# Kernel optimization log

Measured on AMD Instinct MI355X. Metric: run time of the kernel, lower is better.

## Reference

```python
import jax, jax.numpy as jnp
from jax import lax
import numpy as np

B, T = 128, 270
NS = 8            # non-spatial features per step
IH = IW = 64      # spatial precip map
H_LSTM = 256
POOL = 4


def setup_inputs() -> dict:
    key = jax.random.key(0)
    ks = jax.random.split(key, 16)
    r = lambda k, s, sc=0.05: (jax.random.normal(k, s, dtype=jnp.float32) * sc)
    return {
        "x": jax.random.normal(ks[0], (B, T, NS + IH * IW), dtype=jnp.float32),
        "conv1_w": r(ks[1], (2, 1, 3, 3), 0.3),
        "conv1_b": r(ks[2], (2,)),
        "conv2_w": r(ks[3], (4, 2, 3, 3), 0.3),
        "conv2_b": r(ks[4], (4,)),
        "fc_w": r(ks[5], (8, 36), 0.2),
        "fc_b": r(ks[6], (8,)),
        "w_ih": r(ks[7], (4 * H_LSTM, NS + 8), 0.2),
        "w_hh": r(ks[8], (4 * H_LSTM, H_LSTM), 0.06),
        "b_ih": r(ks[9], (4 * H_LSTM,)),
        "b_hh": r(ks[10], (4 * H_LSTM,)),
        "head_w": r(ks[11], (1, H_LSTM), 0.06),
        "head_b": r(ks[12], (1,)),
        "h0": jax.random.normal(ks[13], (B, H_LSTM), dtype=jnp.float32),
        "c0": jax.random.normal(ks[14], (B, H_LSTM), dtype=jnp.float32),
    }


def _conv(z, w, b):
    y = lax.conv_general_dilated(z, w, (1, 1), "VALID",
                                 dimension_numbers=("NCHW", "OIHW", "NCHW"))
    return y + b[None, :, None, None]


def _maxpool(z):
    return lax.reduce_window(z, -jnp.inf, lax.max,
                             (1, 1, POOL, POOL), (1, 1, POOL, POOL), "VALID")


def reference(x, conv1_w, conv1_b, conv2_w, conv2_b, fc_w, fc_b,
              w_ih, w_hh, b_ih, b_hh, head_w, head_b, h0, c0):
    bsz = x.shape[0]
    xs = jnp.swapaxes(x, 0, 1)  # [T, B, NS + IH*IW]

    def step(carry, xt):
        h, c = carry
        x_sp = xt[:, NS:].reshape(bsz, 1, IH, IW)   # spatial precip map
        x_ns = xt[:, :NS]                           # non-spatial features
        o = _maxpool(jax.nn.relu(_conv(x_sp, conv1_w, conv1_b)))
        o = _maxpool(jax.nn.relu(_conv(o, conv2_w, conv2_b)))
        o = o.reshape(bsz, -1) @ fc_w.T + fc_b      # [B, 8]
        inp = jnp.concatenate([x_ns, o], axis=1)    # [B, NS+8]
        gates = inp @ w_ih.T + b_ih + h @ w_hh.T + b_hh  # [B, 4H]
        i, f, g, og = jnp.split(gates, 4, axis=1)   # torch LSTMCell gate order
        c_new = jax.nn.sigmoid(f) * c + jax.nn.sigmoid(i) * jnp.tanh(g)
        h_new = jax.nn.sigmoid(og) * jnp.tanh(c_new)
        return (h_new, c_new), h_new

    _, hs = lax.scan(step, (h0, c0), xs)            # hs: [T, B, H]
    out = jnp.swapaxes(hs, 0, 1) @ head_w.T + head_b  # [B, T, 1]; dropout = eval mode
    return out
```

## Files before the change

kernel.cpp:

```cpp
#include <hip/hip_runtime.h>

#define B_ 128
#define T_ 270
#define XR 4104
#define H_ 256

typedef __attribute__((ext_vector_type(8))) short short8v;
typedef __attribute__((ext_vector_type(4))) float f32x4;

__device__ inline unsigned short f2bf(float f) {
  unsigned u = __builtin_bit_cast(unsigned, f);
  u += 0x7fffu + ((u >> 16) & 1u);
  return (unsigned short)(u >> 16);
}
__device__ inline float sigm(float x) { return 1.0f / (1.0f + __expf(-x)); }
__device__ inline float tanh_f(float x) {
  float t = __expf(-2.0f * fabsf(x));
  float r = (1.0f - t) / (1.0f + t);
  return copysignf(r, x);
}
__device__ inline short8v pack8(const float* p) {
  float4 a = *(const float4*)p, b = *(const float4*)(p + 4);
  short8v v;
  v[0] = (short)f2bf(a.x); v[1] = (short)f2bf(a.y);
  v[2] = (short)f2bf(a.z); v[3] = (short)f2bf(a.w);
  v[4] = (short)f2bf(b.x); v[5] = (short)f2bf(b.y);
  v[6] = (short)f2bf(b.z); v[7] = (short)f2bf(b.w);
  return v;
}
__device__ inline short8v pinned(short8v v) {
  union { short8v s; float f[4]; } u;
  u.s = v;
  asm volatile("" : "+v"(u.f[0]), "+v"(u.f[1]), "+v"(u.f[2]), "+v"(u.f[3]));
  return u.s;
}
#define MFMA(a, b, c) __builtin_amdgcn_mfma_f32_16x16x32_bf16((a), (b), (c), 0, 0, 0)

#define FEAT16_B ((size_t)T_ * B_ * 16 * 2)
#define SPACK_B  ((size_t)8 * 8 * 9 * 64 * 8 * 2)
#define HB_B     ((size_t)2 * 16 * 16 * 128 * 2)
#define HP_B     ((size_t)2 * 16 * 16 * 4 * 4)
#define FLAGS_B  ((size_t)16 * 16 * 4)
#define WS_NEED  (FEAT16_B + SPACK_B + HB_B + HP_B + FLAGS_B)

__global__ __launch_bounds__(256) void cnn_kernel(
    const float* __restrict__ x,
    const float* __restrict__ c1w_, const float* __restrict__ c1b_,
    const float* __restrict__ c2w_, const float* __restrict__ c2b_,
    const float* __restrict__ fcw, const float* __restrict__ fcb,
    unsigned short* __restrict__ feat16, unsigned* __restrict__ flags)
{
  __shared__ float img[64 * 68];
  __shared__ float p1[2 * 15 * 16];
  __shared__ float p2[36];
  __shared__ float wsm[96];
  const int tid = threadIdx.x;
  const int bt = blockIdx.x;
  const int b = bt & 127, t = bt >> 7;

  if (bt == 0 && tid < 16)
    __hip_atomic_store(flags + tid * 16, 0u, __ATOMIC_RELAXED, __HIP_MEMORY_SCOPE_AGENT);

  const float* src = x + ((long)b * T_ + t) * XR;

  if (tid < 18) wsm[tid] = c1w_[tid];
  else if (tid < 20) wsm[tid] = c1b_[tid - 18];
  else if (tid < 92) wsm[tid] = c2w_[tid - 20];
  else if (tid < 96) wsm[tid] = c2b_[tid - 92];

  {
    const float4* s4 = (const float4*)(src + 8);
#pragma unroll
    for (int i0 = 0; i0 < 4; i0++) {
      int i = tid + i0 * 256;
      float4 v = s4[i];
      int e = i * 4;
      *((float4*)&img[(e >> 6) * 68 + (e & 63)]) = v;
    }
  }
  __syncthreads();

  if (tid < 225) {
    int py = tid / 15, px = tid - (tid / 15) * 15;
    float w0[9], w1[9];
#pragma unroll
    for (int j = 0; j < 9; j++) { w0[j] = wsm[j]; w1[j] = wsm[9 + j]; }
    const float b0 = wsm[18], b1v = wsm[19];
    float m0 = -1e30f, m1 = -1e30f;
    for (int dy = 0; dy < 4; dy++) {
      for (int dx = 0; dx < 4; dx++) {
        const float* ip = &img[(py * 4 + dy) * 68 + px * 4 + dx];
        float s0 = b0, s1 = b1v;
#pragma unroll
        for (int ky = 0; ky < 3; ky++) {
#pragma unroll
          for (int kx = 0; kx < 3; kx++) {
            float v = ip[ky * 68 + kx];
            s0 = fmaf(v, w0[ky * 3 + kx], s0);
            s1 = fmaf(v, w1[ky * 3 + kx], s1);
          }
        }
        m0 = fmaxf(m0, s0); m1 = fmaxf(m1, s1);
      }
    }
    p1[py * 16 + px] = fmaxf(m0, 0.f);
    p1[240 + py * 16 + px] = fmaxf(m1, 0.f);
  }
  __syncthreads();

  if (tid < 36) {
    int ch = tid / 9, rem = tid - ch * 9;
    int py = rem / 3, px = rem - py * 3;
    float m = -1e30f;
    for (int dy = 0; dy < 4; dy++) {
      for (int dx = 0; dx < 4; dx++) {
        int y = py * 4 + dy, xx = px * 4 + dx;
        float s = wsm[92 + ch];
#pragma unroll
        for (int ic = 0; ic < 2; ic++)
#pragma unroll
          for (int ky = 0; ky < 3; ky++)
#pragma unroll
            for (int kx = 0; kx < 3; kx++)
              s = fmaf(p1[ic * 240 + (y + ky) * 16 + xx + kx],
                       wsm[20 + ((ch * 2 + ic) * 3 + ky) * 3 + kx], s);
        m = fmaxf(m, s);
      }
    }
    p2[tid] = fmaxf(m, 0.f);
  }
  __syncthreads();

  unsigned short* fr = feat16 + ((long)t * B_ + b) * 16;
  if (tid < 8) {
    float s = fcb[tid];
#pragma unroll
    for (int j = 0; j < 36; j++) s = fmaf(p2[j], fcw[tid * 36 + j], s);
    fr[8 + tid] = f2bf(s);
  } else if (tid < 16) {
    fr[tid - 8] = f2bf(src[tid - 8]);
  }
}

__global__ __launch_bounds__(256) void pack_kernel(
    const float* __restrict__ whh, const float* __restrict__ wih,
    unsigned short* __restrict__ spack)
{
  const int idx = blockIdx.x * 256 + threadIdx.x;
  if (idx >= 8 * 8 * 9 * 64) return;
  const int lane = idx & 63;
  const int fragid = idx >> 6;
  const int s = fragid % 9;
  const int uw = fragid / 9;
  const int u = uw & 7;
  const int hw_ = uw >> 3;
  const int hbk = hw_ >> 2, w = hw_ & 3;
  const int col15 = lane & 15, ko8 = (lane >> 4) * 8;
  const int col = (u >> 1) * 256 + hbk * 128 + w * 32 + (u & 1) * 16 + col15;
  short8v v = {0, 0, 0, 0, 0, 0, 0, 0};
  if (s < 8) {
    const int kf = (s < 4) ? (4 * hbk + s) : (4 * (1 - hbk) + (s - 4));
    v = pack8(whh + col * 256 + kf * 32 + ko8);
  } else if (ko8 < 16) {
    v = pack8(wih + col * 16 + ko8);
  }
  *(short8v*)(spack + (size_t)idx * 8) = v;
}

__global__ __launch_bounds__(256, 1) void lstm_kernel(
    const unsigned short* __restrict__ feat16,
    const float* __restrict__ bih, const float* __restrict__ bhh,
    const float* __restrict__ h0, const float* __restrict__ c0,
    const float* __restrict__ hw, const float* __restrict__ hdb,
    const unsigned short* __restrict__ spack,
    unsigned short* hb16, float* hpg, unsigned* flags,
    float* __restrict__ out)
{
  __shared__ __attribute__((aligned(16))) unsigned short hls[16 * 136];
  __shared__ float hpw[4 * 16];
  const int tid = threadIdx.x;
  const int w = tid >> 6, lane = tid & 63;
  const int gb = blockIdx.x & 7, hbk = blockIdx.x >> 3;
  const int gid = gb * 2 + hbk, pgid = gb * 2 + (1 - hbk);
  const int R0 = gb * 16, D0 = hbk * 128;
  const int col15 = lane & 15, ko8 = (lane >> 4) * 8, rb = (lane >> 4) * 4;
  const int Dl = w * 32;
  const int ar = col15;

  unsigned short* hbB[2] = { hb16, hb16 + 32768 };

  const unsigned short* sbase =
      spack + (size_t)((hbk * 4 + w) * 8) * 9 * 512 + (size_t)lane * 8;
#define SFRAG(u, s) (*(const short8v*)(sbase + ((u) * 9 + (s)) * 512))
  short8v bfO[4][8], bfP[4][8], bfF[8];
#pragma unroll
  for (int u = 0; u < 8; u++) {
#pragma unroll
    for (int s = 0; s < 4; s++) bfO[s][u] = pinned(SFRAG(u, s));
#pragma unroll
    for (int s = 0; s < 4; s++) bfP[s][u] = pinned(SFRAG(u, 4 + s));
    bfF[u] = pinned(SFRAG(u, 8));
  }

  float bsr[8];
#pragma unroll
  for (int u = 0; u < 8; u++) {
    const int col = (u >> 1) * 256 + D0 + Dl + (u & 1) * 16 + col15;
    bsr[u] = bih[col] + bhh[col];
  }
  float hwr[2] = { hw[D0 + Dl + col15], hw[D0 + Dl + 16 + col15] };
  const float hdb0 = hdb[0];

  float cs[2][4];
#pragma unroll
  for (int q = 0; q < 2; q++)
#pragma unroll
    for (int rr = 0; rr < 4; rr++) {
      const int row = rb + rr, dloc = Dl + q * 16 + col15;
      cs[q][rr] = c0[(R0 + row) * H_ + D0 + dloc];
      unsigned short hv = f2bf(h0[(R0 + row) * H_ + D0 + dloc]);
      hls[row * 136 + dloc] = hv;
      __hip_atomic_store(hbB[0] + (gid * 16 + row) * 128 + dloc, hv,
                         __ATOMIC_RELAXED, __HIP_MEMORY_SCOPE_AGENT);
    }
  __syncthreads();
  if (tid == 0)
    __hip_atomic_store(flags + gid * 16, 1u, __ATOMIC_RELEASE, __HIP_MEMORY_SCOPE_AGENT);

  const unsigned* pflag = flags + pgid * 16;

  for (int t = 0; t < T_; t++) {
    short8v af8 = (short8v){0, 0, 0, 0, 0, 0, 0, 0};
    if (ko8 < 16)
      af8 = *(const short8v*)(feat16 + ((size_t)t * B_ + R0 + ar) * 16 + ko8);

    f32x4 acc[8];
#pragma unroll
    for (int u = 0; u < 8; u++) acc[u] = (f32x4){0.f, 0.f, 0.f, 0.f};
#pragma unroll
    for (int s = 0; s < 4; s++) {
      short8v a = *(const short8v*)&hls[ar * 136 + s * 32 + ko8];
#pragma unroll
      for (int u = 0; u < 8; u++) acc[u] = MFMA(a, bfO[s][u], acc[u]);
    }
#pragma unroll
    for (int u = 0; u < 8; u++) acc[u] = MFMA(af8, bfF[u], acc[u]);

    {
      const unsigned need = (unsigned)(t + 1);
      unsigned v; long guard = 0;
      do {
        v = __hip_atomic_load(pflag, __ATOMIC_RELAXED, __HIP_MEMORY_SCOPE_AGENT);
      } while (v < need && ++guard < (1L << 22));
      __builtin_amdgcn_fence(__ATOMIC_ACQUIRE, "agent");
    }

    if (hbk == 0 && tid < 16 && t > 0) {
      float s = hdb0 + hpw[tid] + hpw[16 + tid] + hpw[32 + tid] + hpw[48 + tid];
      const float* pp = hpg + (t & 1) * 1024 + pgid * 64 + tid * 4;
#pragma unroll
      for (int i = 0; i < 4; i++)
        s += __hip_atomic_load(pp + i, __ATOMIC_RELAXED, __HIP_MEMORY_SCOPE_AGENT);
      out[(long)(R0 + tid) * T_ + (t - 1)] = s;
    }

    const unsigned long long* hbr = (const unsigned long long*)hbB[t & 1];
    unsigned long long pq[8];
#pragma unroll
    for (int s = 0; s < 4; s++) {
      const unsigned long long* pr =
          hbr + (size_t)(pgid * 16 + ar) * 32 + s * 8 + (ko8 >> 2);
      pq[2 * s]     = __hip_atomic_load(pr,     __ATOMIC_RELAXED, __HIP_MEMORY_SCOPE_AGENT);
      pq[2 * s + 1] = __hip_atomic_load(pr + 1, __ATOMIC_RELAXED, __HIP_MEMORY_SCOPE_AGENT);
    }
#pragma unroll
    for (int s = 0; s < 4; s++) {
      union { unsigned long long q[2]; short8v v; } u_;
      u_.q[0] = pq[2 * s]; u_.q[1] = pq[2 * s + 1];
#pragma unroll
      for (int u = 0; u < 8; u++) acc[u] = MFMA(u_.v, bfP[s][u], acc[u]);
    }

    __syncthreads();

    unsigned short* hbw = hbB[(t + 1) & 1];
    float ps[4] = {0.f, 0.f, 0.f, 0.f};
#pragma unroll
    for (int q = 0; q < 2; q++)
#pragma unroll
      for (int rr = 0; rr < 4; rr++) {
        float i_ = acc[0 + q][rr] + bsr[0 + q];
        float f_ = acc[2 + q][rr] + bsr[2 + q];
        float g_ = acc[4 + q][rr] + bsr[4 + q];
        float o_ = acc[6 + q][rr] + bsr[6 + q];
        float cn = sigm(f_) * cs[q][rr] + sigm(i_) * tanh_f(g_);
        cs[q][rr] = cn;
        float hn = sigm(o_) * tanh_f(cn);
        const int row = rb + rr, dloc = Dl + q * 16 + col15;
        unsigned short hv = f2bf(hn);
        hls[row * 136 + dloc] = hv;
        __hip_atomic_store(hbw + (gid * 16 + row) * 128 + dloc, hv,
                           __ATOMIC_RELAXED, __HIP_MEMORY_SCOPE_AGENT);
        ps[rr] += hn * hwr[q];
      }
#pragma unroll
    for (int off = 1; off <= 8; off <<= 1)
#pragma unroll
      for (int rr = 0; rr < 4; rr++) ps[rr] += __shfl_xor(ps[rr], off);
    if (col15 == 0) {
#pragma unroll
      for (int rr = 0; rr < 4; rr++) {
        hpw[w * 16 + rb + rr] = ps[rr];
        __hip_atomic_store(hpg + ((t + 1) & 1) * 1024 + gid * 64 + (rb + rr) * 4 + w,
                           ps[rr], __ATOMIC_RELAXED, __HIP_MEMORY_SCOPE_AGENT);
      }
    }

    __syncthreads();
    if (tid == 0)
      __hip_atomic_store(flags + gid * 16, (unsigned)(t + 2),
                         __ATOMIC_RELEASE, __HIP_MEMORY_SCOPE_AGENT);
  }

  if (hbk == 0) {
    {
      const unsigned need = (unsigned)(T_ + 1);
      unsigned v; long guard = 0;
      do {
        v = __hip_atomic_load(pflag, __ATOMIC_RELAXED, __HIP_MEMORY_SCOPE_AGENT);
      } while (v < need && ++guard < (1L << 22));
      __builtin_amdgcn_fence(__ATOMIC_ACQUIRE, "agent");
    }
    if (tid < 16) {
      float s = hdb0 + hpw[tid] + hpw[16 + tid] + hpw[32 + tid] + hpw[48 + tid];
      const float* pp = hpg + (T_ & 1) * 1024 + pgid * 64 + tid * 4;
#pragma unroll
      for (int i = 0; i < 4; i++)
        s += __hip_atomic_load(pp + i, __ATOMIC_RELAXED, __HIP_MEMORY_SCOPE_AGENT);
      out[(long)(R0 + tid) * T_ + (T_ - 1)] = s;
    }
  }
}

extern "C" void kernel_launch(void* const* d_in, const int* in_sizes, int n_in,
                              void* d_out, int out_size, void* d_ws, size_t ws_size,
                              hipStream_t stream) {
  const float* x   = (const float*)d_in[0];
  const float* c1w = (const float*)d_in[1];
  const float* c1b = (const float*)d_in[2];
  const float* c2w = (const float*)d_in[3];
  const float* c2b = (const float*)d_in[4];
  const float* fcw = (const float*)d_in[5];
  const float* fcb = (const float*)d_in[6];
  const float* wih = (const float*)d_in[7];
  const float* whh = (const float*)d_in[8];
  const float* bih = (const float*)d_in[9];
  const float* bhh = (const float*)d_in[10];
  const float* hw  = (const float*)d_in[11];
  const float* hdb = (const float*)d_in[12];
  const float* h0  = (const float*)d_in[13];
  const float* c0  = (const float*)d_in[14];
  float* out = (float*)d_out;

  if (ws_size < WS_NEED) return;
  char* ws = (char*)d_ws;
  unsigned short* feat16 = (unsigned short*)ws;
  unsigned short* spack  = (unsigned short*)(ws + FEAT16_B);
  unsigned short* hb16   = (unsigned short*)(ws + FEAT16_B + SPACK_B);
  float* hpg             = (float*)(ws + FEAT16_B + SPACK_B + HB_B);
  unsigned* flags        = (unsigned*)(ws + FEAT16_B + SPACK_B + HB_B + HP_B);

  cnn_kernel<<<dim3(B_ * T_), dim3(256), 0, stream>>>(
      x, c1w, c1b, c2w, c2b, fcw, fcb, feat16, flags);
  pack_kernel<<<dim3(144), dim3(256), 0, stream>>>(whh, wih, spack);
  lstm_kernel<<<dim3(16), dim3(256), 0, stream>>>(
      feat16, bih, bhh, h0, c0, hw, hdb, spack, hb16, hpg, flags, out);
}
```

Before: 1.457 ms.

## Use per-wave release flags for cross-block LSTM handoff and pin weights in AGPRs

```diff
diff --git a/kernel.cpp b/kernel.cpp
--- a/kernel.cpp
+++ b/kernel.cpp
@@ -34,13 +34,19 @@
   asm volatile("" : "+v"(u.f[0]), "+v"(u.f[1]), "+v"(u.f[2]), "+v"(u.f[3]));
   return u.s;
 }
+__device__ inline short8v pinned_a(short8v v) {
+  union { short8v s; float f[4]; } u;
+  u.s = v;
+  asm volatile("" : "+a"(u.f[0]), "+a"(u.f[1]), "+a"(u.f[2]), "+a"(u.f[3]));
+  return u.s;
+}
 #define MFMA(a, b, c) __builtin_amdgcn_mfma_f32_16x16x32_bf16((a), (b), (c), 0, 0, 0)
 
 #define FEAT16_B ((size_t)T_ * B_ * 16 * 2)
 #define SPACK_B  ((size_t)8 * 8 * 9 * 64 * 8 * 2)
 #define HB_B     ((size_t)2 * 16 * 16 * 128 * 2)
 #define HP_B     ((size_t)2 * 16 * 16 * 4 * 4)
-#define FLAGS_B  ((size_t)16 * 16 * 4)
+#define FLAGS_B  ((size_t)64 * 16 * 4)
 #define WS_NEED  (FEAT16_B + SPACK_B + HB_B + HP_B + FLAGS_B)
 
 __global__ __launch_bounds__(256) void cnn_kernel(
@@ -58,7 +64,7 @@
   const int bt = blockIdx.x;
   const int b = bt & 127, t = bt >> 7;
 
-  if (bt == 0 && tid < 16)
+  if (bt == 0 && tid < 64)
     __hip_atomic_store(flags + tid * 16, 0u, __ATOMIC_RELAXED, __HIP_MEMORY_SCOPE_AGENT);
 
   const float* src = x + ((long)b * T_ + t) * XR;
@@ -196,7 +202,7 @@
 #pragma unroll
   for (int u = 0; u < 8; u++) {
 #pragma unroll
-    for (int s = 0; s < 4; s++) bfO[s][u] = pinned(SFRAG(u, s));
+    for (int s = 0; s < 4; s++) bfO[s][u] = pinned_a(SFRAG(u, s));
 #pragma unroll
     for (int s = 0; s < 4; s++) bfP[s][u] = pinned(SFRAG(u, 4 + s));
     bfF[u] = pinned(SFRAG(u, 8));
@@ -223,11 +229,10 @@
       __hip_atomic_store(hbB[0] + (gid * 16 + row) * 128 + dloc, hv,
                          __ATOMIC_RELAXED, __HIP_MEMORY_SCOPE_AGENT);
     }
+  if (lane == 0)
+    __hip_atomic_store(flags + (gid * 4 + w) * 16, 1u,
+                       __ATOMIC_RELEASE, __HIP_MEMORY_SCOPE_AGENT);
   __syncthreads();
-  if (tid == 0)
-    __hip_atomic_store(flags + gid * 16, 1u, __ATOMIC_RELEASE, __HIP_MEMORY_SCOPE_AGENT);
-
-  const unsigned* pflag = flags + pgid * 16;
 
   for (int t = 0; t < T_; t++) {
     short8v af8 = (short8v){0, 0, 0, 0, 0, 0, 0, 0};
@@ -248,10 +253,14 @@
 
     {
       const unsigned need = (unsigned)(t + 1);
-      unsigned v; long guard = 0;
+      const unsigned* pp = flags + (pgid * 4 + (lane & 3)) * 16;
+      bool ok; long guard = 0;
       do {
-        v = __hip_atomic_load(pflag, __ATOMIC_RELAXED, __HIP_MEMORY_SCOPE_AGENT);
-      } while (v < need && ++guard < (1L << 22));
+        unsigned v = (lane < 4)
+            ? __hip_atomic_load(pp, __ATOMIC_RELAXED, __HIP_MEMORY_SCOPE_AGENT)
+            : need;
+        ok = __all((int)(v >= need));
+      } while (!ok && ++guard < (1L << 22));
       __builtin_amdgcn_fence(__ATOMIC_ACQUIRE, "agent");
     }
 
@@ -316,19 +325,23 @@
       }
     }
 
+    if (lane == 0)
+      __hip_atomic_store(flags + (gid * 4 + w) * 16, (unsigned)(t + 2),
+                         __ATOMIC_RELEASE, __HIP_MEMORY_SCOPE_AGENT);
     __syncthreads();
-    if (tid == 0)
-      __hip_atomic_store(flags + gid * 16, (unsigned)(t + 2),
-                         __ATOMIC_RELEASE, __HIP_MEMORY_SCOPE_AGENT);
   }
 
   if (hbk == 0) {
     {
       const unsigned need = (unsigned)(T_ + 1);
-      unsigned v; long guard = 0;
+      const unsigned* pp = flags + (pgid * 4 + (lane & 3)) * 16;
+      bool ok; long guard = 0;
       do {
-        v = __hip_atomic_load(pflag, __ATOMIC_RELAXED, __HIP_MEMORY_SCOPE_AGENT);
-      } while (v < need && ++guard < (1L << 22));
+        unsigned v = (lane < 4)
+            ? __hip_atomic_load(pp, __ATOMIC_RELAXED, __HIP_MEMORY_SCOPE_AGENT)
+            : need;
+        ok = __all((int)(v >= need));
+      } while (!ok && ++guard < (1L << 22));
       __builtin_amdgcn_fence(__ATOMIC_ACQUIRE, "agent");
     }
     if (tid < 16) {
```

Result: no change. 1.452 ms (-0.3%).

## Process two batch row-groups per LSTM block to overlap partner-wait with compute

Applied to the files above, without the earlier changes.

```diff
diff --git a/kernel.cpp b/kernel.cpp
--- a/kernel.cpp
+++ b/kernel.cpp
@@ -34,13 +34,19 @@
   asm volatile("" : "+v"(u.f[0]), "+v"(u.f[1]), "+v"(u.f[2]), "+v"(u.f[3]));
   return u.s;
 }
+__device__ inline short8v pinned_a(short8v v) {
+  union { short8v s; float f[4]; } u;
+  u.s = v;
+  asm volatile("" : "+a"(u.f[0]), "+a"(u.f[1]), "+a"(u.f[2]), "+a"(u.f[3]));
+  return u.s;
+}
 #define MFMA(a, b, c) __builtin_amdgcn_mfma_f32_16x16x32_bf16((a), (b), (c), 0, 0, 0)
 
 #define FEAT16_B ((size_t)T_ * B_ * 16 * 2)
 #define SPACK_B  ((size_t)8 * 8 * 9 * 64 * 8 * 2)
 #define HB_B     ((size_t)2 * 16 * 16 * 128 * 2)
 #define HP_B     ((size_t)2 * 16 * 16 * 4 * 4)
-#define FLAGS_B  ((size_t)16 * 16 * 4)
+#define FLAGS_B  ((size_t)8 * 16 * 4)
 #define WS_NEED  (FEAT16_B + SPACK_B + HB_B + HP_B + FLAGS_B)
 
 __global__ __launch_bounds__(256) void cnn_kernel(
@@ -58,7 +64,7 @@
   const int bt = blockIdx.x;
   const int b = bt & 127, t = bt >> 7;
 
-  if (bt == 0 && tid < 16)
+  if (bt == 0 && tid < 8)
     __hip_atomic_store(flags + tid * 16, 0u, __ATOMIC_RELAXED, __HIP_MEMORY_SCOPE_AGENT);
 
   const float* src = x + ((long)b * T_ + t) * XR;
@@ -154,12 +160,12 @@
   const int uw = fragid / 9;
   const int u = uw & 7;
   const int hw_ = uw >> 3;
-  const int hbk = hw_ >> 2, w = hw_ & 3;
+  const int half = hw_ >> 2, w = hw_ & 3;
   const int col15 = lane & 15, ko8 = (lane >> 4) * 8;
-  const int col = (u >> 1) * 256 + hbk * 128 + w * 32 + (u & 1) * 16 + col15;
+  const int col = (u >> 1) * 256 + half * 128 + w * 32 + (u & 1) * 16 + col15;
   short8v v = {0, 0, 0, 0, 0, 0, 0, 0};
   if (s < 8) {
-    const int kf = (s < 4) ? (4 * hbk + s) : (4 * (1 - hbk) + (s - 4));
+    const int kf = (s < 4) ? (4 * half + s) : (4 * (1 - half) + (s - 4));
     v = pack8(whh + col * 256 + kf * 32 + ko8);
   } else if (ko8 < 16) {
     v = pack8(wih + col * 16 + ko8);
@@ -176,29 +182,33 @@
     unsigned short* hb16, float* hpg, unsigned* flags,
     float* __restrict__ out)
 {
-  __shared__ __attribute__((aligned(16))) unsigned short hls[16 * 136];
-  __shared__ float hpw[4 * 16];
+  __shared__ __attribute__((aligned(16))) unsigned short hlsA[16 * 136];
+  __shared__ __attribute__((aligned(16))) unsigned short hlsB[16 * 136];
+  __shared__ float headpA[64], headpB[64];
+
   const int tid = threadIdx.x;
   const int w = tid >> 6, lane = tid & 63;
-  const int gb = blockIdx.x & 7, hbk = blockIdx.x >> 3;
-  const int gid = gb * 2 + hbk, pgid = gb * 2 + (1 - hbk);
-  const int R0 = gb * 16, D0 = hbk * 128;
+  const int q = blockIdx.x & 3, half = blockIdx.x >> 2;
+  const int gidA = 4 * q + half,     pgidA = 4 * q + (1 - half);
+  const int gidB = 4 * q + 2 + half, pgidB = 4 * q + 2 + (1 - half);
+  const int R0A = q * 32, R0B = q * 32 + 16;
+  const int D0 = half * 128, Dl = w * 32;
   const int col15 = lane & 15, ko8 = (lane >> 4) * 8, rb = (lane >> 4) * 4;
-  const int Dl = w * 32;
   const int ar = col15;
-
-  unsigned short* hbB[2] = { hb16, hb16 + 32768 };
+  const int pblk = blockIdx.x ^ 4;
+
+  unsigned short* hbB2[2] = { hb16, hb16 + 32768 };
 
   const unsigned short* sbase =
-      spack + (size_t)((hbk * 4 + w) * 8) * 9 * 512 + (size_t)lane * 8;
+      spack + (size_t)((half * 4 + w) * 8) * 9 * 512 + (size_t)lane * 8;
 #define SFRAG(u, s) (*(const short8v*)(sbase + ((u) * 9 + (s)) * 512))
   short8v bfO[4][8], bfP[4][8], bfF[8];
 #pragma unroll
   for (int u = 0; u < 8; u++) {
 #pragma unroll
-    for (int s = 0; s < 4; s++) bfO[s][u] = pinned(SFRAG(u, s));
-#pragma unroll
-    for (int s = 0; s < 4; s++) bfP[s][u] = pinned(SFRAG(u, 4 + s));
+    for (int s = 0; s < 4; s++) bfO[s][u] = pinned_a(SFRAG(u, s));
+#pragma unroll
+    for (int s = 0; s < 4; s++) bfP[s][u] = pinned_a(SFRAG(u, 4 + s));
     bfF[u] = pinned(SFRAG(u, 8));
   }
 
@@ -211,41 +221,31 @@
   float hwr[2] = { hw[D0 + Dl + col15], hw[D0 + Dl + 16 + col15] };
   const float hdb0 = hdb[0];
 
-  float cs[2][4];
-#pragma unroll
-  for (int q = 0; q < 2; q++)
+  float csA[2][4], csB[2][4];
+#pragma unroll
+  for (int q2 = 0; q2 < 2; q2++)
 #pragma unroll
     for (int rr = 0; rr < 4; rr++) {
-      const int row = rb + rr, dloc = Dl + q * 16 + col15;
-      cs[q][rr] = c0[(R0 + row) * H_ + D0 + dloc];
-      unsigned short hv = f2bf(h0[(R0 + row) * H_ + D0 + dloc]);
-      hls[row * 136 + dloc] = hv;
-      __hip_atomic_store(hbB[0] + (gid * 16 + row) * 128 + dloc, hv,
+      const int row = rb + rr, dloc = Dl + q2 * 16 + col15;
+      csA[q2][rr] = c0[(R0A + row) * H_ + D0 + dloc];
+      csB[q2][rr] = c0[(R0B + row) * H_ + D0 + dloc];
+      unsigned short hvA = f2bf(h0[(R0A + row) * H_ + D0 + dloc]);
+      unsigned short hvB = f2bf(h0[(R0B + row) * H_ + D0 + dloc]);
+      hlsA[row * 136 + dloc] = hvA;
+      hlsB[row * 136 + dloc] = hvB;
+      __hip_atomic_store(hbB2[0] + (gidA * 16 + row) * 128 + dloc, hvA,
+                         __ATOMIC_RELAXED, __HIP_MEMORY_SCOPE_AGENT);
+      __hip_atomic_store(hbB2[0] + (gidB * 16 + row) * 128 + dloc, hvB,
                          __ATOMIC_RELAXED, __HIP_MEMORY_SCOPE_AGENT);
     }
   __syncthreads();
   if (tid == 0)
-    __hip_atomic_store(flags + gid * 16, 1u, __ATOMIC_RELEASE, __HIP_MEMORY_SCOPE_AGENT);
-
-  const unsigned* pflag = flags + pgid * 16;
+    __hip_atomic_store(flags + blockIdx.x * 16, 1u,
+                       __ATOMIC_RELEASE, __HIP_MEMORY_SCOPE_AGENT);
+
+  const unsigned* pflag = flags + pblk * 16;
 
   for (int t = 0; t < T_; t++) {
-    short8v af8 = (short8v){0, 0, 0, 0, 0, 0, 0, 0};
-    if (ko8 < 16)
-      af8 = *(const short8v*)(feat16 + ((size_t)t * B_ + R0 + ar) * 16 + ko8);
-
-    f32x4 acc[8];
-#pragma unroll
-    for (int u = 0; u < 8; u++) acc[u] = (f32x4){0.f, 0.f, 0.f, 0.f};
-#pragma unroll
-    for (int s = 0; s < 4; s++) {
-      short8v a = *(const short8v*)&hls[ar * 136 + s * 32 + ko8];
-#pragma unroll
-      for (int u = 0; u < 8; u++) acc[u] = MFMA(a, bfO[s][u], acc[u]);
-    }
-#pragma unroll
-    for (int u = 0; u < 8; u++) acc[u] = MFMA(af8, bfF[u], acc[u]);
-
     {
       const unsigned need = (unsigned)(t + 1);
       unsigned v; long guard = 0;
@@ -255,74 +255,175 @@
       __builtin_amdgcn_fence(__ATOMIC_ACQUIRE, "agent");
     }
 
-    if (hbk == 0 && tid < 16 && t > 0) {
-      float s = hdb0 + hpw[tid] + hpw[16 + tid] + hpw[32 + tid] + hpw[48 + tid];
-      const float* pp = hpg + (t & 1) * 1024 + pgid * 64 + tid * 4;
-#pragma unroll
-      for (int i = 0; i < 4; i++)
-        s += __hip_atomic_load(pp + i, __ATOMIC_RELAXED, __HIP_MEMORY_SCOPE_AGENT);
-      out[(long)(R0 + tid) * T_ + (t - 1)] = s;
-    }
-
-    const unsigned long long* hbr = (const unsigned long long*)hbB[t & 1];
-    unsigned long long pq[8];
+    const unsigned long long* hbr = (const unsigned long long*)hbB2[t & 1];
+    unsigned long long pqA[8];
 #pragma unroll
     for (int s = 0; s < 4; s++) {
       const unsigned long long* pr =
-          hbr + (size_t)(pgid * 16 + ar) * 32 + s * 8 + (ko8 >> 2);
-      pq[2 * s]     = __hip_atomic_load(pr,     __ATOMIC_RELAXED, __HIP_MEMORY_SCOPE_AGENT);
-      pq[2 * s + 1] = __hip_atomic_load(pr + 1, __ATOMIC_RELAXED, __HIP_MEMORY_SCOPE_AGENT);
-    }
-#pragma unroll
-    for (int s = 0; s < 4; s++) {
-      union { unsigned long long q[2]; short8v v; } u_;
-      u_.q[0] = pq[2 * s]; u_.q[1] = pq[2 * s + 1];
-#pragma unroll
-      for (int u = 0; u < 8; u++) acc[u] = MFMA(u_.v, bfP[s][u], acc[u]);
+          hbr + (size_t)(pgidA * 16 + ar) * 32 + s * 8 + (ko8 >> 2);
+      pqA[2 * s]     = __hip_atomic_load(pr,     __ATOMIC_RELAXED, __HIP_MEMORY_SCOPE_AGENT);
+      pqA[2 * s + 1] = __hip_atomic_load(pr + 1, __ATOMIC_RELAXED, __HIP_MEMORY_SCOPE_AGENT);
+    }
+    short8v afA = (short8v){0, 0, 0, 0, 0, 0, 0, 0};
+    short8v afB = (short8v){0, 0, 0, 0, 0, 0, 0, 0};
+    if (ko8 < 16) {
+      afA = *(const short8v*)(feat16 + ((size_t)t * B_ + R0A + ar) * 16 + ko8);
+      afB = *(const short8v*)(feat16 + ((size_t)t * B_ + R0B + ar) * 16 + ko8);
+    }
+    float hp0 = 0.f, hp1 = 0.f, hp2 = 0.f, hp3 = 0.f;
+    if (half == 0 && t > 0) {
+      const float* pp = nullptr;
+      if (tid < 16)                 pp = hpg + (t & 1) * 1024 + pgidA * 64 + tid * 4;
+      else if (tid >= 64 && tid < 80) pp = hpg + (t & 1) * 1024 + pgidB * 64 + (tid - 64) * 4;
+      if (pp) {
+        hp0 = __hip_atomic_load(pp + 0, __ATOMIC_RELAXED, __HIP_MEMORY_SCOPE_AGENT);
+        hp1 = __hip_atomic_load(pp + 1, __ATOMIC_RELAXED, __HIP_MEMORY_SCOPE_AGENT);
+        hp2 = __hip_atomic_load(pp + 2, __ATOMIC_RELAXED, __HIP_MEMORY_SCOPE_AGENT);
+        hp3 = __hip_atomic_load(pp + 3, __ATOMIC_RELAXED, __HIP_MEMORY_SCOPE_AGENT);
+      }
+    }
+
+    f32x4 accA[8], accB[8];
+#pragma unroll
+    for (int u = 0; u < 8; u++) accA[u] = (f32x4){0.f, 0.f, 0.f, 0.f};
+#pragma unroll
+    for (int u = 0; u < 8; u++) accB[u] = (f32x4){0.f, 0.f, 0.f, 0.f};
+#pragma unroll
+    for (int s = 0; s < 4; s++) {
+      short8v a = *(const short8v*)&hlsA[ar * 136 + s * 32 + ko8];
+#pragma unroll
+      for (int u = 0; u < 8; u++) accA[u] = MFMA(a, bfO[s][u], accA[u]);
+    }
+#pragma unroll
+    for (int u = 0; u < 8; u++) accA[u] = MFMA(afA, bfF[u], accA[u]);
+#pragma unroll
+    for (int s = 0; s < 4; s++) {
+      short8v a = *(const short8v*)&hlsB[ar * 136 + s * 32 + ko8];
+#pragma unroll
+      for (int u = 0; u < 8; u++) accB[u] = MFMA(a, bfO[s][u], accB[u]);
+    }
+#pragma unroll
+    for (int u = 0; u < 8; u++) accB[u] = MFMA(afB, bfF[u], accB[u]);
+
+    float hsum = 0.f;
+    if (half == 0 && t > 0) {
+      if (tid < 16)
+        hsum = headpA[tid] + headpA[16 + tid] + headpA[32 + tid] + headpA[48 + tid];
+      else if (tid >= 64 && tid < 80) {
+        int r = tid - 64;
+        hsum = headpB[r] + headpB[16 + r] + headpB[32 + r] + headpB[48 + r];
+      }
     }
 
     __syncthreads();
 
-    unsigned short* hbw = hbB[(t + 1) & 1];
-    float ps[4] = {0.f, 0.f, 0.f, 0.f};
-#pragma unroll
-    for (int q = 0; q < 2; q++)
-#pragma unroll
-      for (int rr = 0; rr < 4; rr++) {
-        float i_ = acc[0 + q][rr] + bsr[0 + q];
-        float f_ = acc[2 + q][rr] + bsr[2 + q];
-        float g_ = acc[4 + q][rr] + bsr[4 + q];
-        float o_ = acc[6 + q][rr] + bsr[6 + q];
-        float cn = sigm(f_) * cs[q][rr] + sigm(i_) * tanh_f(g_);
-        cs[q][rr] = cn;
-        float hn = sigm(o_) * tanh_f(cn);
-        const int row = rb + rr, dloc = Dl + q * 16 + col15;
-        unsigned short hv = f2bf(hn);
-        hls[row * 136 + dloc] = hv;
-        __hip_atomic_store(hbw + (gid * 16 + row) * 128 + dloc, hv,
-                           __ATOMIC_RELAXED, __HIP_MEMORY_SCOPE_AGENT);
-        ps[rr] += hn * hwr[q];
-      }
-#pragma unroll
-    for (int off = 1; off <= 8; off <<= 1)
-#pragma unroll
-      for (int rr = 0; rr < 4; rr++) ps[rr] += __shfl_xor(ps[rr], off);
-    if (col15 == 0) {
-#pragma unroll
-      for (int rr = 0; rr < 4; rr++) {
-        hpw[w * 16 + rb + rr] = ps[rr];
-        __hip_atomic_store(hpg + ((t + 1) & 1) * 1024 + gid * 64 + (rb + rr) * 4 + w,
-                           ps[rr], __ATOMIC_RELAXED, __HIP_MEMORY_SCOPE_AGENT);
-      }
+    if (half == 0 && t > 0) {
+      if (tid < 16)
+        out[(long)(R0A + tid) * T_ + (t - 1)] = hdb0 + hsum + hp0 + hp1 + hp2 + hp3;
+      else if (tid >= 64 && tid < 80)
+        out[(long)(R0B + (tid - 64)) * T_ + (t - 1)] = hdb0 + hsum + hp0 + hp1 + hp2 + hp3;
+    }
+
+    unsigned long long pqB[8];
+#pragma unroll
+    for (int s = 0; s < 4; s++) {
+      const unsigned long long* pr =
+          hbr + (size_t)(pgidB * 16 + ar) * 32 + s * 8 + (ko8 >> 2);
+      pqB[2 * s]     = __hip_atomic_load(pr,     __ATOMIC_RELAXED, __HIP_MEMORY_SCOPE_AGENT);
+      pqB[2 * s + 1] = __hip_atomic_load(pr + 1, __ATOMIC_RELAXED, __HIP_MEMORY_SCOPE_AGENT);
+    }
+
+#pragma unroll
+    for (int s = 0; s < 4; s++) {
+      union { unsigned long long qv[2]; short8v v; } u_;
+      u_.qv[0] = pqA[2 * s]; u_.qv[1] = pqA[2 * s + 1];
+#pragma unroll
+      for (int u = 0; u < 8; u++) accA[u] = MFMA(u_.v, bfP[s][u], accA[u]);
+    }
+
+    unsigned short* hbw = hbB2[(t + 1) & 1];
+
+    {
+      float ps[4] = {0.f, 0.f, 0.f, 0.f};
+#pragma unroll
+      for (int q2 = 0; q2 < 2; q2++)
+#pragma unroll
+        for (int rr = 0; rr < 4; rr++) {
+          float i_ = accA[0 + q2][rr] + bsr[0 + q2];
+          float f_ = accA[2 + q2][rr] + bsr[2 + q2];
+          float g_ = accA[4 + q2][rr] + bsr[4 + q2];
+          float o_ = accA[6 + q2][rr] + bsr[6 + q2];
+          float cn = sigm(f_) * csA[q2][rr] + sigm(i_) * tanh_f(g_);
+          csA[q2][rr] = cn;
+          float hn = sigm(o_) * tanh_f(cn);
+          const int row = rb + rr, dloc = Dl + q2 * 16 + col15;
+          unsigned short hv = f2bf(hn);
+          hlsA[row * 136 + dloc] = hv;
+          __hip_atomic_store(hbw + (gidA * 16 + row) * 128 + dloc, hv,
+                             __ATOMIC_RELAXED, __HIP_MEMORY_SCOPE_AGENT);
+          ps[rr] += hn * hwr[q2];
+        }
+#pragma unroll
+      for (int off = 1; off <= 8; off <<= 1)
+#pragma unroll
+        for (int rr = 0; rr < 4; rr++) ps[rr] += __shfl_xor(ps[rr], off);
+      if (col15 == 0)
+#pragma unroll
+        for (int rr = 0; rr < 4; rr++) {
+          headpA[w * 16 + rb + rr] = ps[rr];
+          __hip_atomic_store(hpg + ((t + 1) & 1) * 1024 + gidA * 64 + (rb + rr) * 4 + w,
+                             ps[rr], __ATOMIC_RELAXED, __HIP_MEMORY_SCOPE_AGENT);
+        }
+    }
+
+#pragma unroll
+    for (int s = 0; s < 4; s++) {
+      union { unsigned long long qv[2]; short8v v; } u_;
+      u_.qv[0] = pqB[2 * s]; u_.qv[1] = pqB[2 * s + 1];
+#pragma unroll
+      for (int u = 0; u < 8; u++) accB[u] = MFMA(u_.v, bfP[s][u], accB[u]);
+    }
+
+    {
+      float ps[4] = {0.f, 0.f, 0.f, 0.f};
+#pragma unroll
+      for (int q2 = 0; q2 < 2; q2++)
+#pragma unroll
+        for (int rr = 0; rr < 4; rr++) {
+          float i_ = accB[0 + q2][rr] + bsr[0 + q2];
+          float f_ = accB[2 + q2][rr] + bsr[2 + q2];
+          float g_ = accB[4 + q2][rr] + bsr[4 + q2];
+          float o_ = accB[6 + q2][rr] + bsr[6 + q2];
+          float cn = sigm(f_) * csB[q2][rr] + sigm(i_) * tanh_f(g_);
+          csB[q2][rr] = cn;
+          float hn = sigm(o_) * tanh_f(cn);
+          const int row = rb + rr, dloc = Dl + q2 * 16 + col15;
+          unsigned short hv = f2bf(hn);
+          hlsB[row * 136 + dloc] = hv;
+          __hip_atomic_store(hbw + (gidB * 16 + row) * 128 + dloc, hv,
+                             __ATOMIC_RELAXED, __HIP_MEMORY_SCOPE_AGENT);
+          ps[rr] += hn * hwr[q2];
+        }
+#pragma unroll
+      for (int off = 1; off <= 8; off <<= 1)
+#pragma unroll
+        for (int rr = 0; rr < 4; rr++) ps[rr] += __shfl_xor(ps[rr], off);
+      if (col15 == 0)
+#pragma unroll
+        for (int rr = 0; rr < 4; rr++) {
+          headpB[w * 16 + rb + rr] = ps[rr];
+          __hip_atomic_store(hpg + ((t + 1) & 1) * 1024 + gidB * 64 + (rb + rr) * 4 + w,
+                             ps[rr], __ATOMIC_RELAXED, __HIP_MEMORY_SCOPE_AGENT);
+        }
     }
 
     __syncthreads();
     if (tid == 0)
-      __hip_atomic_store(flags + gid * 16, (unsigned)(t + 2),
+      __hip_atomic_store(flags + blockIdx.x * 16, (unsigned)(t + 2),
                          __ATOMIC_RELEASE, __HIP_MEMORY_SCOPE_AGENT);
   }
 
-  if (hbk == 0) {
+  if (half == 0) {
     {
       const unsigned need = (unsigned)(T_ + 1);
       unsigned v; long guard = 0;
@@ -332,12 +433,20 @@
       __builtin_amdgcn_fence(__ATOMIC_ACQUIRE, "agent");
     }
     if (tid < 16) {
-      float s = hdb0 + hpw[tid] + hpw[16 + tid] + hpw[32 + tid] + hpw[48 + tid];
-      const float* pp = hpg + (T_ & 1) * 1024 + pgid * 64 + tid * 4;
+      float s = hdb0 + headpA[tid] + headpA[16 + tid] + headpA[32 + tid] + headpA[48 + tid];
+      const float* pp = hpg + (T_ & 1) * 1024 + pgidA * 64 + tid * 4;
 #pragma unroll
       for (int i = 0; i < 4; i++)
         s += __hip_atomic_load(pp + i, __ATOMIC_RELAXED, __HIP_MEMORY_SCOPE_AGENT);
-      out[(long)(R0 + tid) * T_ + (T_ - 1)] = s;
+      out[(long)(R0A + tid) * T_ + (T_ - 1)] = s;
+    } else if (tid >= 64 && tid < 80) {
+      int r = tid - 64;
+      float s = hdb0 + headpB[r] + headpB[16 + r] + headpB[32 + r] + headpB[48 + r];
+      const float* pp = hpg + (T_ & 1) * 1024 + pgidB * 64 + r * 4;
+#pragma unroll
+      for (int i = 0; i < 4; i++)
+        s += __hip_atomic_load(pp + i, __ATOMIC_RELAXED, __HIP_MEMORY_SCOPE_AGENT);
+      out[(long)(R0B + r) * T_ + (T_ - 1)] = s;
     }
   }
 }
@@ -373,6 +482,6 @@
   cnn_kernel<<<dim3(B_ * T_), dim3(256), 0, stream>>>(
       x, c1w, c1b, c2w, c2b, fcw, fcb, feat16, flags);
   pack_kernel<<<dim3(144), dim3(256), 0, stream>>>(whh, wih, spack);
-  lstm_kernel<<<dim3(16), dim3(256), 0, stream>>>(
+  lstm_kernel<<<dim3(8), dim3(256), 0, stream>>>(
       feat16, bih, bhh, h0, c0, hw, hdb, spack, hb16, hpg, flags, out);
 }
```

Result: slower. 2.099 ms (+44.1%).
